# Optimization experiments

Hardware: AMD Instinct MI355X
Metric: run time of the kernel (lower is better)

## Reference

```python
import jax, jax.numpy as jnp
import numpy as np
import itertools

RANKS_HIGH = 15
SUITS_HIGH = 5
B, M = 16, 24
# Omaha unspool: choose 2 of 4 hole cards x choose 3 of 5 board cards -> 60 five-card combos
COMBOS = np.array([h + b for h in itertools.combinations(range(4), 2)
                   for b in itertools.combinations(range(4, 9), 3)], dtype=np.int32)  # [60, 5]


def setup_inputs() -> dict:
    key = jax.random.key(0)
    ks = list(jax.random.split(key, 20))
    f = lambda i, shape: jax.random.normal(ks[i], shape, jnp.float32) * 0.05
    ranks = jax.random.randint(ks[0], (B, M, 9), 2, RANKS_HIGH)  # card ranks 2..14
    suits = jax.random.randint(ks[1], (B, M, 9), 1, SUITS_HIGH)  # suits 1..4
    x = jnp.stack([ranks, suits], axis=-1).reshape(B, M, 18)     # alternating rank/suit
    ones16 = jnp.ones((16,), jnp.float32)
    zeros16 = jnp.zeros((16,), jnp.float32)
    return {
        "x": x,
        "suit_w": f(2, (16, 5, 1)), "suit_b": f(3, (16,)),
        "rank_w": f(4, (16, 5, 5)), "rank_b": f(5, (16,)),
        "bn_s_gamma": ones16, "bn_s_beta": zeros16, "bn_s_mean": zeros16, "bn_s_var": ones16,
        "bn_r_gamma": ones16, "bn_r_beta": zeros16, "bn_r_mean": zeros16, "bn_r_var": ones16,
        "w1": f(6, (32, 16)), "b1": f(7, (32,)),
        "w2": f(8, (32, 32)), "b2": f(9, (32,)),
        "wc": f(10, (7463, 512)), "bc": f(11, (7463,)),
        "wo1": f(12, (512, 15360)), "bo1": f(13, (512,)),
        "wo2": f(14, (256, 512)), "bo2": f(15, (256,)),
        "wo3": f(16, (127, 256)), "bo3": f(17, (127,)),
    }


def _bn(t, gamma, beta, mean, var, eps=1e-5):
    # eval-mode BatchNorm1d; channel axis is -2 (shape [..., 16, L])
    inv = gamma / jnp.sqrt(var + eps)
    return t * inv[:, None] + (beta - mean * inv)[:, None]


def _forward(x, suit_w, suit_b, bn_s_gamma, bn_s_beta, bn_s_mean, bn_s_var,
             rank_w, rank_b, bn_r_gamma, bn_r_beta, bn_r_mean, bn_r_var,
             w1, b1, w2, b2, wc, bc, wo1, bo1, wo2, bo2, wo3, bo3):
    b, m, _ = x.shape
    ranks = x[..., 0::2][..., COMBOS]  # [B,M,60,5]
    suits = x[..., 1::2][..., COMBOS]  # [B,M,60,5]
    hot_r = jax.nn.one_hot(ranks, RANKS_HIGH, dtype=jnp.float32)  # [B,M,60,5,15]
    hot_s = jax.nn.one_hot(suits, SUITS_HIGH, dtype=jnp.float32)  # [B,M,60,5,5]
    # suit conv: Conv1d(5,16,k=1) over the one-hot length; channels = 5 cards
    s = jnp.einsum('bmkcl,oc->bmkol', hot_s, suit_w[:, :, 0]) + suit_b[:, None]
    s = jax.nn.relu(_bn(s, bn_s_gamma, bn_s_beta, bn_s_mean, bn_s_var))  # [B,M,60,16,5]
    # rank conv: Conv1d(5,16,k=5) valid: length 15 -> 11
    n = b * m * 60
    r = jax.lax.conv_general_dilated(hot_r.reshape(n, 5, RANKS_HIGH), rank_w,
                                     window_strides=(1,), padding='VALID',
                                     dimension_numbers=('NCH', 'OIH', 'NCH'))
    r = r.reshape(b, m, 60, 16, 11) + rank_b[:, None]
    r = jax.nn.relu(_bn(r, bn_r_gamma, bn_r_beta, bn_r_mean, bn_r_var))  # [B,M,60,16,11]
    raw = jnp.concatenate([r, s], axis=-1)  # [B,M,60,16,16]
    # hand-class head: two hidden linears on last dim, then 512 -> 7463
    h = jax.nn.relu(raw @ w1.T + b1)        # [B,M,60,16,32]
    h = jax.nn.relu(h @ w2.T + b2)          # [B,M,60,16,32]
    logits = h.reshape(b, m, 60, 512) @ wc.T + bc  # [B,M,60,7463]
    best = jnp.min(jnp.argmax(jax.lax.stop_gradient(logits), axis=-1),
                   axis=-1, keepdims=True)  # [B,M,1] (lower class index = better hand)
    # raw-feature head: [B,M,60*16*16=15360] -> 512 -> 256 -> 127
    o = raw.reshape(b, m, 60 * 16 * 16)
    o = jax.nn.relu(o @ wo1.T + bo1)
    o = jax.nn.relu(o @ wo2.T + bo2)
    o = jax.nn.relu(o @ wo3.T + bo3)
    return jnp.concatenate([o, best.astype(o.dtype)], axis=-1)  # [B,M,128]


def reference(x, suit_w, suit_b, bn_s_gamma, bn_s_beta, bn_s_mean, bn_s_var,
              rank_w, rank_b, bn_r_gamma, bn_r_beta, bn_r_mean, bn_r_var,
              w1, b1, w2, b2, wc, bc, wo1, bo1, wo2, bo2, wo3, bo3):
    return _forward(x, suit_w, suit_b, bn_s_gamma, bn_s_beta, bn_s_mean, bn_s_var,
                    rank_w, rank_b, bn_r_gamma, bn_r_beta, bn_r_mean, bn_r_var,
                    w1, b1, w2, b2, wc, bc, wo1, bo1, wo2, bo2, wo3, bo3)
```

## Files before the change

### kernel.cpp

```cpp
#include <hip/hip_runtime.h>

#define NSAMP 384
#define NCOMBO 60
#define NROW 23040
#define KDIM 512
#define NCLS 7463
#define NCLSP 7680
#define NTILE_N 30
#define NTILE_M 90
#define O1_NZ 30
#define O1_KZ 512

typedef short s16x8 __attribute__((ext_vector_type(8)));
typedef short s16x4 __attribute__((ext_vector_type(4)));
typedef float f32x4 __attribute__((ext_vector_type(4)));

__device__ unsigned short g_wc_hi[NCLSP * KDIM];
__device__ unsigned short g_wc_lo[NCLSP * KDIM];
__device__ unsigned short g_h_hi[NROW * KDIM];
__device__ unsigned short g_h_lo[NROW * KDIM];
__device__ unsigned short g_rawbf[NROW * 256];
__device__ unsigned short g_wo1bf[512 * 15360];
__device__ float          g_pmax[NTILE_N * NROW];
__device__ int            g_pidx[NTILE_N * NROW];
__device__ float          g_part[O1_NZ * NSAMP * 512];

__device__ __forceinline__ float bf2f(unsigned short u){
  union { unsigned int i; float f; } v; v.i = ((unsigned int)u) << 16; return v.f;
}
__device__ __forceinline__ unsigned short f2bf(float f){
  union { float f; unsigned int i; } v; v.f = f;
  unsigned int u = v.i;
  unsigned int r = (u + 0x7FFFu + ((u >> 16) & 1u)) >> 16;
  return (unsigned short)r;
}
__device__ __forceinline__ void gload16(const void* g, void* l){
  __builtin_amdgcn_global_load_lds((const __attribute__((address_space(1))) void*)g,
                                   (__attribute__((address_space(3))) void*)l, 16, 0, 0);
}

__global__ __launch_bounds__(256) void k_split(const float* __restrict__ wc)
{
  int idx = (blockIdx.x * 256 + threadIdx.x) * 4;
  float4 w = {0.f, 0.f, 0.f, 0.f};
  if (idx < NCLS * KDIM) w = *(const float4*)(wc + idx);
  s16x4 hi, lo;
  float wv[4] = {w.x, w.y, w.z, w.w};
  #pragma unroll
  for (int i = 0; i < 4; ++i){
    unsigned short h = f2bf(wv[i]);
    hi[i] = (short)h;
    lo[i] = (short)f2bf(wv[i] - bf2f(h));
  }
  *(s16x4*)(g_wc_hi + idx) = hi;
  *(s16x4*)(g_wc_lo + idx) = lo;
}

__global__ __launch_bounds__(256) void k_splitw(const float* __restrict__ wo1)
{
  int idx = (blockIdx.x * 256 + threadIdx.x) * 4;
  float4 w = *(const float4*)(wo1 + idx);
  s16x4 b;
  b[0] = (short)f2bf(w.x); b[1] = (short)f2bf(w.y);
  b[2] = (short)f2bf(w.z); b[3] = (short)f2bf(w.w);
  *(s16x4*)(g_wo1bf + idx) = b;
}

__global__ __launch_bounds__(256) void k_features(
    const int* __restrict__ x,
    const float* __restrict__ suit_w, const float* __restrict__ suit_b,
    const float* __restrict__ rank_w, const float* __restrict__ rank_b,
    const float* __restrict__ bns_g, const float* __restrict__ bns_b,
    const float* __restrict__ bns_m, const float* __restrict__ bns_v,
    const float* __restrict__ bnr_g, const float* __restrict__ bnr_b,
    const float* __restrict__ bnr_m, const float* __restrict__ bnr_v,
    const float* __restrict__ w1, const float* __restrict__ b1,
    const float* __restrict__ w2, const float* __restrict__ b2)
{
  __shared__ float raw_s[4][256];
  __shared__ float h1_s[4][512];
  const int tid  = threadIdx.x;
  const int lane = tid & 63;
  const int wv   = tid >> 6;
  const int combo = blockIdx.x * 4 + wv;
  const int s = combo / 60;
  const int k = combo % 60;
  const int hp = k / 10, bt = k % 10;
  const int HP0[6]  = {0,0,0,1,1,2}, HP1[6] = {1,2,3,2,3,3};
  const int BT0[10] = {4,4,4,4,4,4,5,5,5,6};
  const int BT1[10] = {5,5,5,6,6,7,6,6,7,7};
  const int BT2[10] = {6,7,8,7,8,8,7,8,8,8};
  int cards[5] = {HP0[hp], HP1[hp], BT0[bt], BT1[bt], BT2[bt]};
  const int* xp = x + s * 18;
  int rk[5], st[5];
  #pragma unroll
  for (int c = 0; c < 5; ++c){ rk[c] = xp[2*cards[c]]; st[c] = xp[2*cards[c] + 1]; }

  {
    s16x4 rv;
    #pragma unroll
    for (int i = 0; i < 4; ++i){
      int e = lane * 4 + i;
      int o = e >> 4, l = e & 15;
      float v;
      if (l < 11){
        float a = 0.f;
        #pragma unroll
        for (int c = 0; c < 5; ++c){
          int d = rk[c] - l;
          if (d >= 0 && d < 5) a += rank_w[o*25 + c*5 + d];
        }
        a += rank_b[o];
        float inv = bnr_g[o] / sqrtf(bnr_v[o] + 1e-5f);
        v = a * inv + (bnr_b[o] - bnr_m[o] * inv);
      } else {
        int j = l - 11;
        float a = suit_b[o];
        #pragma unroll
        for (int c = 0; c < 5; ++c) if (st[c] == j) a += suit_w[o*5 + c];
        float inv = bns_g[o] / sqrtf(bns_v[o] + 1e-5f);
        v = a * inv + (bns_b[o] - bns_m[o] * inv);
      }
      v = fmaxf(v, 0.f);
      raw_s[wv][e] = v;
      rv[i] = (short)f2bf(v);
    }
    *(s16x4*)(g_rawbf + (size_t)s * 15360 + k * 256 + lane * 4) = rv;
  }
  __syncthreads();
  #pragma unroll
  for (int i = 0; i < 8; ++i){
    int e = lane + 64 * i;
    int o = e >> 5, j = e & 31;
    float a = b1[j];
    #pragma unroll
    for (int l = 0; l < 16; ++l) a += raw_s[wv][o*16 + l] * w1[j*16 + l];
    h1_s[wv][e] = fmaxf(a, 0.f);
  }
  __syncthreads();
  {
    s16x8 hv, lv;
    #pragma unroll
    for (int i = 0; i < 8; ++i){
      int e = lane * 8 + i;
      int o = e >> 5, j = e & 31;
      float a = b2[j];
      #pragma unroll
      for (int l = 0; l < 32; ++l) a += h1_s[wv][o*32 + l] * w2[j*32 + l];
      a = fmaxf(a, 0.f);
      unsigned short h = f2bf(a);
      hv[i] = (short)h;
      lv[i] = (short)f2bf(a - bf2f(h));
    }
    *(s16x8*)(g_h_hi + (size_t)combo * 512 + lane * 8) = hv;
    *(s16x8*)(g_h_lo + (size_t)combo * 512 + lane * 8) = lv;
  }
}

__global__ __launch_bounds__(512, 2) void k_logits(const float* __restrict__ bc)
{
  __shared__ unsigned char lds[65536];
  const int tid  = threadIdx.x;
  const int lane = tid & 63;
  const int wv   = tid >> 6;
  const int wm   = wv >> 2, wn = wv & 3;
  const int blk  = blockIdx.x;
  const int nt   = blk / NTILE_M;
  const int mt   = blk % NTILE_M;
  const int m0 = mt * 256;
  const int n0 = nt * 256;

  f32x4 acc[8][4];
  #pragma unroll
  for (int i = 0; i < 8; ++i)
    #pragma unroll
    for (int j = 0; j < 4; ++j)
      acc[i][j] = (f32x4){0.f, 0.f, 0.f, 0.f};

  const int sR0 = tid >> 2;
  const int sCS = (tid & 3) ^ ((tid >> 3) & 3);
  auto stage = [&](int buf, int t){
    const int seg = t >> 4;
    const int kc  = (t & 15) * 32;
    const unsigned short* As = (seg < 2) ? g_h_hi : g_h_lo;
    const unsigned short* Bs = (seg == 1) ? g_wc_lo : g_wc_hi;
    const unsigned base = buf * 32768;
    #pragma unroll
    for (int it = 0; it < 2; ++it){
      int R = it * 128 + sR0;
      gload16(As + (size_t)(m0 + R) * KDIM + kc + sCS * 8,
              lds + base + it * 8192 + wv * 1024);
    }
    #pragma unroll
    for (int it = 0; it < 2; ++it){
      int R = it * 128 + sR0;
      gload16(Bs + (size_t)(n0 + R) * KDIM + kc + sCS * 8,
              lds + base + 16384 + it * 8192 + wv * 1024);
    }
  };

  stage(0, 0);
  stage(1, 1);
  asm volatile("s_waitcnt vmcnt(4)" ::: "memory");
  __builtin_amdgcn_sched_barrier(0);
  __builtin_amdgcn_s_barrier();
  asm volatile("" ::: "memory");

  const int q = lane >> 4;
  #pragma unroll 1
  for (int t = 0; t < 48; ++t){
    const unsigned cb = (unsigned)(t & 1) * 32768;
    s16x8 af[8], bf[4];
    #pragma unroll
    for (int i = 0; i < 8; ++i){
      int row = wm * 128 + i * 16 + (lane & 15);
      af[i] = *(const s16x8*)(lds + cb + row * 64 + ((q ^ ((row >> 1) & 3)) << 4));
    }
    #pragma unroll
    for (int j = 0; j < 4; ++j){
      int row = wn * 64 + j * 16 + (lane & 15);
      bf[j] = *(const s16x8*)(lds + cb + 16384 + row * 64 + ((q ^ ((row >> 1) & 3)) << 4));
    }
    __builtin_amdgcn_s_setprio(1);
    #pragma unroll
    for (int i = 0; i < 8; ++i)
      #pragma unroll
      for (int j = 0; j < 4; ++j)
        acc[i][j] = __builtin_amdgcn_mfma_f32_16x16x32_bf16(af[i], bf[j], acc[i][j], 0, 0, 0);
    __builtin_amdgcn_s_setprio(0);
    __builtin_amdgcn_sched_barrier(0);
    __builtin_amdgcn_s_barrier();
    asm volatile("" ::: "memory");
    if (t + 2 < 48){
      stage(t & 1, t + 2);
      asm volatile("s_waitcnt vmcnt(4)" ::: "memory");
    } else {
      asm volatile("s_waitcnt vmcnt(0)" ::: "memory");
    }
    __builtin_amdgcn_sched_barrier(0);
    __builtin_amdgcn_s_barrier();
    asm volatile("" ::: "memory");
  }

  float* cmax = (float*)lds;
  int*   cidx = (int*)(lds + 4096);
  const int g = lane >> 4;
  #pragma unroll
  for (int i = 0; i < 8; ++i){
    #pragma unroll
    for (int r = 0; r < 4; ++r){
      float bv = -__builtin_inff(); int bi = 0x7FFFFFFF;
      #pragma unroll
      for (int j = 0; j < 4; ++j){
        int col = n0 + wn * 64 + j * 16 + (lane & 15);
        if (col < NCLS){
          float v = acc[i][j][r] + bc[col];
          if (v > bv){ bv = v; bi = col; }
        }
      }
      for (int s = 1; s < 16; s <<= 1){
        float ov = __shfl_xor(bv, s);
        int   oi = __shfl_xor(bi, s);
        if (ov > bv || (ov == bv && oi < bi)){ bv = ov; bi = oi; }
      }
      if ((lane & 15) == 0){
        int rloc = wm * 128 + i * 16 + g * 4 + r;
        cmax[rloc * 4 + wn] = bv;
        cidx[rloc * 4 + wn] = bi;
      }
    }
  }
  __syncthreads();
  if (tid < 256){
    float bv = cmax[tid * 4]; int bi = cidx[tid * 4];
    #pragma unroll
    for (int wq = 1; wq < 4; ++wq){
      float v = cmax[tid * 4 + wq]; int i1 = cidx[tid * 4 + wq];
      if (v > bv || (v == bv && i1 < bi)){ bv = v; bi = i1; }
    }
    size_t row = (size_t)(m0 + tid);
    g_pmax[(size_t)nt * NROW + row] = bv;
    g_pidx[(size_t)nt * NROW + row] = bi;
  }
}

__global__ __launch_bounds__(64) void k_best(float* __restrict__ out)
{
  __shared__ int bis[60];
  const int s = blockIdx.x; const int t = threadIdx.x;
  if (t < 60){
    size_t row = (size_t)s * 60 + t;
    float bv = -__builtin_inff(); int bi = 0x7FFFFFFF;
    for (int q = 0; q < NTILE_N; ++q){
      float v = g_pmax[(size_t)q * NROW + row];
      int   i = g_pidx[(size_t)q * NROW + row];
      if (v > bv || (v == bv && i < bi)){ bv = v; bi = i; }
    }
    bis[t] = bi;
  }
  __syncthreads();
  if (t == 0){
    int m = bis[0];
    for (int i = 1; i < 60; ++i) m = min(m, bis[i]);
    out[s * 128 + 127] = (float)m;
  }
}

__global__ __launch_bounds__(256) void k_o1(void)
{
  __shared__ unsigned char As[16384];
  __shared__ unsigned char Bs[16384];
  const int tid  = threadIdx.x;
  const int lane = tid & 63;
  const int wv   = tid >> 6;
  const int wr   = wv >> 1, wq = wv & 1;
  const int n0  = blockIdx.x * 128;
  const int m0  = blockIdx.y * 128;
  const int kc0 = blockIdx.z * O1_KZ;

  f32x4 acc[4][4];
  #pragma unroll
  for (int i = 0; i < 4; ++i)
    #pragma unroll
    for (int j = 0; j < 4; ++j)
      acc[i][j] = (f32x4){0.f, 0.f, 0.f, 0.f};

  const int rA = lane >> 3;
  const int c0 = lane & 7;
  for (int kk = 0; kk < O1_KZ; kk += 64){
    int kc = kc0 + kk;
    __syncthreads();
    #pragma unroll
    for (int it = 0; it < 4; ++it){
      int seg = wv * 4 + it;
      int r   = seg * 8 + rA;
      int cs  = c0 ^ (r & 7);
      gload16(g_rawbf + (size_t)(m0 + r) * 15360 + kc + cs * 8, As + seg * 1024);
      gload16(g_wo1bf + (size_t)(n0 + r) * 15360 + kc + cs * 8, Bs + seg * 1024);
    }
    __syncthreads();
    #pragma unroll
    for (int ks = 0; ks < 2; ++ks){
      int q = ks * 4 + (lane >> 4);
      s16x8 a[4];
      #pragma unroll
      for (int i = 0; i < 4; ++i){
        int row = wr * 64 + i * 16 + (lane & 15);
        a[i] = *(const s16x8*)(As + row * 128 + ((q ^ (row & 7)) * 16));
      }
      #pragma unroll
      for (int j = 0; j < 4; ++j){
        int col = wq * 64 + j * 16 + (lane & 15);
        s16x8 b = *(const s16x8*)(Bs + col * 128 + ((q ^ (col & 7)) * 16));
        #pragma unroll
        for (int i = 0; i < 4; ++i)
          acc[i][j] = __builtin_amdgcn_mfma_f32_16x16x32_bf16(a[i], b, acc[i][j], 0, 0, 0);
      }
    }
  }
  const int g = lane >> 4;
  #pragma unroll
  for (int i = 0; i < 4; ++i)
    #pragma unroll
    for (int j = 0; j < 4; ++j)
      #pragma unroll
      for (int r = 0; r < 4; ++r){
        int gm = m0 + wr * 64 + i * 16 + g * 4 + r;
        int gn = n0 + wq * 64 + j * 16 + (lane & 15);
        g_part[((size_t)blockIdx.z * NSAMP + gm) * 512 + gn] = acc[i][j][r];
      }
}

__global__ __launch_bounds__(256) void k_otail(
    const float* __restrict__ bo1, const float* __restrict__ wo2,
    const float* __restrict__ bo2, const float* __restrict__ wo3,
    const float* __restrict__ bo3, float* __restrict__ out)
{
  __shared__ float o1f[512];
  __shared__ float o2f[256];
  const int s = blockIdx.x;
  const int tid = threadIdx.x;
  for (int j = tid; j < 512; j += 256){
    float a = bo1[j];
    for (int ks = 0; ks < O1_NZ; ++ks) a += g_part[((size_t)ks * NSAMP + s) * 512 + j];
    o1f[j] = fmaxf(a, 0.f);
  }
  __syncthreads();
  {
    float a = bo2[tid];
    const float* wr = wo2 + (size_t)tid * 512;
    for (int i = 0; i < 512; i += 4){
      float4 w4 = *(const float4*)(wr + i);
      a += o1f[i]*w4.x + o1f[i+1]*w4.y + o1f[i+2]*w4.z + o1f[i+3]*w4.w;
    }
    o2f[tid] = fmaxf(a, 0.f);
  }
  __syncthreads();
  if (tid < 127){
    float a = bo3[tid];
    const float* wr = wo3 + (size_t)tid * 256;
    for (int i = 0; i < 256; i += 4){
      float4 w4 = *(const float4*)(wr + i);
      a += o2f[i]*w4.x + o2f[i+1]*w4.y + o2f[i+2]*w4.z + o2f[i+3]*w4.w;
    }
    out[s * 128 + tid] = fmaxf(a, 0.f);
  }
}

extern "C" void kernel_launch(void* const* d_in, const int* in_sizes, int n_in,
                              void* d_out, int out_size, void* d_ws, size_t ws_size,
                              hipStream_t stream)
{
  (void)d_ws; (void)ws_size; (void)in_sizes; (void)n_in; (void)out_size;
  const int*   x      = (const int*)  d_in[0];
  const float* suit_w = (const float*)d_in[1];
  const float* suit_b = (const float*)d_in[2];
  const float* rank_w = (const float*)d_in[3];
  const float* rank_b = (const float*)d_in[4];
  const float* bns_g  = (const float*)d_in[5];
  const float* bns_b  = (const float*)d_in[6];
  const float* bns_m  = (const float*)d_in[7];
  const float* bns_v  = (const float*)d_in[8];
  const float* bnr_g  = (const float*)d_in[9];
  const float* bnr_b  = (const float*)d_in[10];
  const float* bnr_m  = (const float*)d_in[11];
  const float* bnr_v  = (const float*)d_in[12];
  const float* w1     = (const float*)d_in[13];
  const float* b1     = (const float*)d_in[14];
  const float* w2     = (const float*)d_in[15];
  const float* b2     = (const float*)d_in[16];
  const float* wc     = (const float*)d_in[17];
  const float* bc     = (const float*)d_in[18];
  const float* wo1    = (const float*)d_in[19];
  const float* bo1    = (const float*)d_in[20];
  const float* wo2    = (const float*)d_in[21];
  const float* bo2    = (const float*)d_in[22];
  const float* wo3    = (const float*)d_in[23];
  const float* bo3    = (const float*)d_in[24];
  float* out = (float*)d_out;

  hipLaunchKernelGGL(k_split,  dim3(3840), dim3(256), 0, stream, wc);
  hipLaunchKernelGGL(k_splitw, dim3(7680), dim3(256), 0, stream, wo1);
  hipLaunchKernelGGL(k_features, dim3(5760), dim3(256), 0, stream, x,
                     suit_w, suit_b, rank_w, rank_b,
                     bns_g, bns_b, bns_m, bns_v, bnr_g, bnr_b, bnr_m, bnr_v,
                     w1, b1, w2, b2);
  hipLaunchKernelGGL(k_logits, dim3(NTILE_N * NTILE_M), dim3(512), 0, stream, bc);
  hipLaunchKernelGGL(k_best, dim3(NSAMP), dim3(64), 0, stream, out);
  hipLaunchKernelGGL(k_o1, dim3(4, 3, O1_NZ), dim3(256), 0, stream);
  hipLaunchKernelGGL(k_otail, dim3(NSAMP), dim3(256), 0, stream,
                     bo1, wo2, bo2, wo3, bo3, out);
}
```

Measured before the change: 1.156 ms.

## Halve logits GEMM M-tile for higher occupancy and fuse small kernels

The logits GEMM now uses 128x256 tiles with 48KB LDS and launch bounds allowing 4 blocks per CU, instead of 256x256 tiles at 2 blocks. The three-segment split-bf16 K loop is interleaved per K chunk. Separately, the two weight-conversion kernels are merged into one launch, and the best-class reduction is folded into the tail kernel to remove launches. The smaller tiles lower reuse of the B operand per loaded byte, trading extra memory traffic for latency hiding.

```diff
diff --git a/kernel.cpp b/kernel.cpp
--- a/kernel.cpp
+++ b/kernel.cpp
@@ -7,7 +7,7 @@
 #define NCLS 7463
 #define NCLSP 7680
 #define NTILE_N 30
-#define NTILE_M 90
+#define NTILE_M 180
 #define O1_NZ 30
 #define O1_KZ 512
 
@@ -39,31 +39,32 @@
                                    (__attribute__((address_space(3))) void*)l, 16, 0, 0);
 }
 
-__global__ __launch_bounds__(256) void k_split(const float* __restrict__ wc)
-{
-  int idx = (blockIdx.x * 256 + threadIdx.x) * 4;
-  float4 w = {0.f, 0.f, 0.f, 0.f};
-  if (idx < NCLS * KDIM) w = *(const float4*)(wc + idx);
-  s16x4 hi, lo;
-  float wv[4] = {w.x, w.y, w.z, w.w};
-  #pragma unroll
-  for (int i = 0; i < 4; ++i){
-    unsigned short h = f2bf(wv[i]);
-    hi[i] = (short)h;
-    lo[i] = (short)f2bf(wv[i] - bf2f(h));
-  }
-  *(s16x4*)(g_wc_hi + idx) = hi;
-  *(s16x4*)(g_wc_lo + idx) = lo;
-}
-
-__global__ __launch_bounds__(256) void k_splitw(const float* __restrict__ wo1)
-{
-  int idx = (blockIdx.x * 256 + threadIdx.x) * 4;
-  float4 w = *(const float4*)(wo1 + idx);
-  s16x4 b;
-  b[0] = (short)f2bf(w.x); b[1] = (short)f2bf(w.y);
-  b[2] = (short)f2bf(w.z); b[3] = (short)f2bf(w.w);
-  *(s16x4*)(g_wo1bf + idx) = b;
+__global__ __launch_bounds__(256) void k_prep(const float* __restrict__ wc,
+                                              const float* __restrict__ wo1)
+{
+  int b = blockIdx.x;
+  if (b < 3840){
+    int idx = (b * 256 + threadIdx.x) * 4;
+    float4 w = {0.f, 0.f, 0.f, 0.f};
+    if (idx < NCLS * KDIM) w = *(const float4*)(wc + idx);
+    s16x4 hi, lo;
+    float wv[4] = {w.x, w.y, w.z, w.w};
+    #pragma unroll
+    for (int i = 0; i < 4; ++i){
+      unsigned short h = f2bf(wv[i]);
+      hi[i] = (short)h;
+      lo[i] = (short)f2bf(wv[i] - bf2f(h));
+    }
+    *(s16x4*)(g_wc_hi + idx) = hi;
+    *(s16x4*)(g_wc_lo + idx) = lo;
+  } else {
+    int idx = ((b - 3840) * 256 + threadIdx.x) * 4;
+    float4 w = *(const float4*)(wo1 + idx);
+    s16x4 v;
+    v[0] = (short)f2bf(w.x); v[1] = (short)f2bf(w.y);
+    v[2] = (short)f2bf(w.z); v[3] = (short)f2bf(w.w);
+    *(s16x4*)(g_wo1bf + idx) = v;
+  }
 }
 
 __global__ __launch_bounds__(256) void k_features(
@@ -157,9 +158,9 @@
   }
 }
 
-__global__ __launch_bounds__(512, 2) void k_logits(const float* __restrict__ bc)
-{
-  __shared__ unsigned char lds[65536];
+__global__ __launch_bounds__(512, 4) void k_logits(const float* __restrict__ bc)
+{
+  __shared__ unsigned char lds[49152];
   const int tid  = threadIdx.x;
   const int lane = tid & 63;
   const int wv   = tid >> 6;
@@ -167,41 +168,32 @@
   const int blk  = blockIdx.x;
   const int nt   = blk / NTILE_M;
   const int mt   = blk % NTILE_M;
-  const int m0 = mt * 256;
+  const int m0 = mt * 128;
   const int n0 = nt * 256;
 
-  f32x4 acc[8][4];
-  #pragma unroll
-  for (int i = 0; i < 8; ++i)
+  f32x4 acc[4][4];
+  #pragma unroll
+  for (int i = 0; i < 4; ++i)
     #pragma unroll
     for (int j = 0; j < 4; ++j)
       acc[i][j] = (f32x4){0.f, 0.f, 0.f, 0.f};
 
-  const int sR0 = tid >> 2;
-  const int sCS = (tid & 3) ^ ((tid >> 3) & 3);
+  const int rS = wv * 16 + (lane >> 2);
+  const int cS = (lane & 3) ^ ((lane >> 3) & 3);
   auto stage = [&](int buf, int t){
-    const int seg = t >> 4;
-    const int kc  = (t & 15) * 32;
+    const int p = t / 3, seg = t - p * 3;
+    const int kc = p * 32;
     const unsigned short* As = (seg < 2) ? g_h_hi : g_h_lo;
     const unsigned short* Bs = (seg == 1) ? g_wc_lo : g_wc_hi;
-    const unsigned base = buf * 32768;
-    #pragma unroll
-    for (int it = 0; it < 2; ++it){
-      int R = it * 128 + sR0;
-      gload16(As + (size_t)(m0 + R) * KDIM + kc + sCS * 8,
-              lds + base + it * 8192 + wv * 1024);
-    }
-    #pragma unroll
-    for (int it = 0; it < 2; ++it){
-      int R = it * 128 + sR0;
-      gload16(Bs + (size_t)(n0 + R) * KDIM + kc + sCS * 8,
-              lds + base + 16384 + it * 8192 + wv * 1024);
-    }
+    const unsigned base = buf * 24576 + wv * 1024;
+    gload16(As + (size_t)(m0 + rS) * KDIM + kc + cS * 8, lds + base);
+    gload16(Bs + (size_t)(n0 + rS) * KDIM + kc + cS * 8, lds + base + 8192);
+    gload16(Bs + (size_t)(n0 + 128 + rS) * KDIM + kc + cS * 8, lds + base + 16384);
   };
 
   stage(0, 0);
   stage(1, 1);
-  asm volatile("s_waitcnt vmcnt(4)" ::: "memory");
+  asm volatile("s_waitcnt vmcnt(3)" ::: "memory");
   __builtin_amdgcn_sched_barrier(0);
   __builtin_amdgcn_s_barrier();
   asm volatile("" ::: "memory");
@@ -209,21 +201,21 @@
   const int q = lane >> 4;
   #pragma unroll 1
   for (int t = 0; t < 48; ++t){
-    const unsigned cb = (unsigned)(t & 1) * 32768;
-    s16x8 af[8], bf[4];
-    #pragma unroll
-    for (int i = 0; i < 8; ++i){
-      int row = wm * 128 + i * 16 + (lane & 15);
+    const unsigned cb = (unsigned)(t & 1) * 24576;
+    s16x8 af[4], bf[4];
+    #pragma unroll
+    for (int i = 0; i < 4; ++i){
+      int row = wm * 64 + i * 16 + (lane & 15);
       af[i] = *(const s16x8*)(lds + cb + row * 64 + ((q ^ ((row >> 1) & 3)) << 4));
     }
     #pragma unroll
     for (int j = 0; j < 4; ++j){
       int row = wn * 64 + j * 16 + (lane & 15);
-      bf[j] = *(const s16x8*)(lds + cb + 16384 + row * 64 + ((q ^ ((row >> 1) & 3)) << 4));
+      bf[j] = *(const s16x8*)(lds + cb + 8192 + row * 64 + ((q ^ ((row >> 1) & 3)) << 4));
     }
     __builtin_amdgcn_s_setprio(1);
     #pragma unroll
-    for (int i = 0; i < 8; ++i)
+    for (int i = 0; i < 4; ++i)
       #pragma unroll
       for (int j = 0; j < 4; ++j)
         acc[i][j] = __builtin_amdgcn_mfma_f32_16x16x32_bf16(af[i], bf[j], acc[i][j], 0, 0, 0);
@@ -233,7 +225,7 @@
     asm volatile("" ::: "memory");
     if (t + 2 < 48){
       stage(t & 1, t + 2);
-      asm volatile("s_waitcnt vmcnt(4)" ::: "memory");
+      asm volatile("s_waitcnt vmcnt(3)" ::: "memory");
     } else {
       asm volatile("s_waitcnt vmcnt(0)" ::: "memory");
     }
@@ -243,10 +235,10 @@
   }
 
   float* cmax = (float*)lds;
-  int*   cidx = (int*)(lds + 4096);
+  int*   cidx = (int*)(lds + 2048);
   const int g = lane >> 4;
   #pragma unroll
-  for (int i = 0; i < 8; ++i){
+  for (int i = 0; i < 4; ++i){
     #pragma unroll
     for (int r = 0; r < 4; ++r){
       float bv = -__builtin_inff(); int bi = 0x7FFFFFFF;
@@ -264,14 +256,14 @@
         if (ov > bv || (ov == bv && oi < bi)){ bv = ov; bi = oi; }
       }
       if ((lane & 15) == 0){
-        int rloc = wm * 128 + i * 16 + g * 4 + r;
+        int rloc = wm * 64 + i * 16 + g * 4 + r;
         cmax[rloc * 4 + wn] = bv;
         cidx[rloc * 4 + wn] = bi;
       }
     }
   }
   __syncthreads();
-  if (tid < 256){
+  if (tid < 128){
     float bv = cmax[tid * 4]; int bi = cidx[tid * 4];
     #pragma unroll
     for (int wq = 1; wq < 4; ++wq){
@@ -281,28 +273,6 @@
     size_t row = (size_t)(m0 + tid);
     g_pmax[(size_t)nt * NROW + row] = bv;
     g_pidx[(size_t)nt * NROW + row] = bi;
-  }
-}
-
-__global__ __launch_bounds__(64) void k_best(float* __restrict__ out)
-{
-  __shared__ int bis[60];
-  const int s = blockIdx.x; const int t = threadIdx.x;
-  if (t < 60){
-    size_t row = (size_t)s * 60 + t;
-    float bv = -__builtin_inff(); int bi = 0x7FFFFFFF;
-    for (int q = 0; q < NTILE_N; ++q){
-      float v = g_pmax[(size_t)q * NROW + row];
-      int   i = g_pidx[(size_t)q * NROW + row];
-      if (v > bv || (v == bv && i < bi)){ bv = v; bi = i; }
-    }
-    bis[t] = bi;
-  }
-  __syncthreads();
-  if (t == 0){
-    int m = bis[0];
-    for (int i = 1; i < 60; ++i) m = min(m, bis[i]);
-    out[s * 128 + 127] = (float)m;
   }
 }
 
@@ -371,15 +341,26 @@
       }
 }
 
-__global__ __launch_bounds__(256) void k_otail(
+__global__ __launch_bounds__(256) void k_tail(
     const float* __restrict__ bo1, const float* __restrict__ wo2,
     const float* __restrict__ bo2, const float* __restrict__ wo3,
     const float* __restrict__ bo3, float* __restrict__ out)
 {
   __shared__ float o1f[512];
   __shared__ float o2f[256];
+  __shared__ int   bis[60];
   const int s = blockIdx.x;
   const int tid = threadIdx.x;
+  if (tid < 60){
+    size_t row = (size_t)s * 60 + tid;
+    float bv = -__builtin_inff(); int bi = 0x7FFFFFFF;
+    for (int qn = 0; qn < NTILE_N; ++qn){
+      float v = g_pmax[(size_t)qn * NROW + row];
+      int   i = g_pidx[(size_t)qn * NROW + row];
+      if (v > bv || (v == bv && i < bi)){ bv = v; bi = i; }
+    }
+    bis[tid] = bi;
+  }
   for (int j = tid; j < 512; j += 256){
     float a = bo1[j];
     for (int ks = 0; ks < O1_NZ; ++ks) a += g_part[((size_t)ks * NSAMP + s) * 512 + j];
@@ -404,6 +385,11 @@
       a += o2f[i]*w4.x + o2f[i+1]*w4.y + o2f[i+2]*w4.z + o2f[i+3]*w4.w;
     }
     out[s * 128 + tid] = fmaxf(a, 0.f);
+  }
+  if (tid == 0){
+    int m = bis[0];
+    for (int i = 1; i < 60; ++i) m = min(m, bis[i]);
+    out[s * 128 + 127] = (float)m;
   }
 }
 
@@ -439,15 +425,13 @@
   const float* bo3    = (const float*)d_in[24];
   float* out = (float*)d_out;
 
-  hipLaunchKernelGGL(k_split,  dim3(3840), dim3(256), 0, stream, wc);
-  hipLaunchKernelGGL(k_splitw, dim3(7680), dim3(256), 0, stream, wo1);
+  hipLaunchKernelGGL(k_prep, dim3(11520), dim3(256), 0, stream, wc, wo1);
   hipLaunchKernelGGL(k_features, dim3(5760), dim3(256), 0, stream, x,
                      suit_w, suit_b, rank_w, rank_b,
                      bns_g, bns_b, bns_m, bns_v, bnr_g, bnr_b, bnr_m, bnr_v,
                      w1, b1, w2, b2);
   hipLaunchKernelGGL(k_logits, dim3(NTILE_N * NTILE_M), dim3(512), 0, stream, bc);
-  hipLaunchKernelGGL(k_best, dim3(NSAMP), dim3(64), 0, stream, out);
   hipLaunchKernelGGL(k_o1, dim3(4, 3, O1_NZ), dim3(256), 0, stream);
-  hipLaunchKernelGGL(k_otail, dim3(NSAMP), dim3(256), 0, stream,
+  hipLaunchKernelGGL(k_tail, dim3(NSAMP), dim3(256), 0, stream,
                      bo1, wo2, bo2, wo3, bo3, out);
 }
```

Result: faster. 1.083 ms (-6.3%).
